# Optimization experiments

Measured on AMD Instinct MI355X. Metric: run time of the kernel, lower is better.

Reference implementation:

```python
import jax, jax.numpy as jnp
import numpy as np

R = 256        # residual channels
SKIP = 256     # skip channels
COND = 80      # conditioning (mel) channels
NUM_CLS = 256  # mu-law classes
T = 1024       # samples to generate
DILATIONS = tuple([1, 2, 4, 8, 16, 32, 64, 128, 256, 512] * 3)  # 30 layers, kernel_size=2
L = len(DILATIONS)


def setup_inputs() -> dict:
    key = jax.random.key(0)
    ks = jax.random.split(key, 15)
    sc = 0.05
    f = jnp.float32
    return {
        "y": jax.random.normal(ks[0], (COND, T), f),
        "emb": jnp.tanh(jax.random.normal(ks[1], (NUM_CLS, R), f)),  # buffer stores emb.tanh()
        "condition_W": jax.random.normal(ks[2], (L * 2 * R, COND), f) * sc,
        "WV_past": jax.random.normal(ks[3], (L, 2 * R, R), f) * sc,      # K=2 -> one past tap
        "WV_present": jax.random.normal(ks[4], (L, 2 * R, R), f) * sc,
        "W_o_weight": jax.random.normal(ks[5], (L - 1, R + SKIP, R), f) * sc,
        "W_o_bias": jax.random.normal(ks[6], (L - 1, R + SKIP), f) * sc,
        "W_o_weight_last": jax.random.normal(ks[7], (SKIP, R), f) * sc,
        "W_o_bias_last": jax.random.normal(ks[8], (SKIP,), f) * sc,
        "end1_w": jax.random.normal(ks[9], (SKIP, SKIP), f) * sc,
        "end1_b": jax.random.normal(ks[10], (SKIP,), f) * sc,
        "end2_w": jax.random.normal(ks[11], (NUM_CLS, SKIP), f) * sc,
        "end2_b": jax.random.normal(ks[12], (NUM_CLS,), f) * sc,
        "samples": jax.random.uniform(ks[13], (T,), f),  # torch.rand(T) inverse-CDF draws
    }


def _generate(y, emb, condition_W, WV_past, WV_present, W_o_weight, W_o_bias,
              W_o_weight_last, W_o_bias_last, end1_w, end1_b, end2_w, end2_b,
              samples, c=1.0):
    # all conditioning projections at once; chunked per layer as in torch.chunk(.., L, dim=0)
    conds_seq = (condition_W @ y).T.reshape(T, L, 2 * R)  # [T, L, 2R]
    x0 = emb[NUM_CLS // 2 - 1]
    mems0 = tuple(jnp.zeros((R, d), y.dtype) for d in DILATIONS)  # ring buffers per layer
    idx0 = jnp.zeros((L,), jnp.int32)

    def step(carry, inp):
        mems, idxs, x = carry
        cond_t, u = inp
        skip = jnp.zeros((SKIP,), x.dtype)
        new_mems, new_idxs = [], []
        for j in range(L):  # fixed small layer loop (structurally distinct buffers)
            mem, idx = mems[j], idxs[j]
            # kernel_size=2 -> single past tap read from ring buffer at idx
            h = cond_t[j] + WV_past[j] @ jnp.take(mem, idx, axis=1) + WV_present[j] @ x
            mem = mem.at[:, idx].set(x)  # write present sample, advance ring pointer
            new_mems.append(mem)
            new_idxs.append((idx + 1) % mem.shape[1])
            zw, zf = jnp.split(h, 2)
            z = jnp.tanh(zw) * jax.nn.sigmoid(zf)  # gated activation
            if j < L - 1:
                z2 = W_o_weight[j] @ z + W_o_bias[j]
                x = x + z2[:R]          # residual
                skip = skip + z2[R:]    # skip accumulation
            else:
                skip = skip + W_o_weight_last @ z + W_o_bias_last
        hid = jax.nn.relu(end1_w @ jax.nn.relu(skip) + end1_b)
        logits = (end2_w @ hid + end2_b) * c
        cum = jnp.cumsum(jax.nn.softmax(logits))
        new_idx = jnp.argmax(cum > u)  # first index with cum-prob > u  (inverse-CDF sample)
        return (tuple(new_mems), jnp.stack(new_idxs), emb[new_idx]), (new_idx, logits)

    _, (outputs, logits) = jax.lax.scan(step, (mems0, idx0, x0), (conds_seq, samples))
    return outputs.astype(jnp.int64), logits


def reference(y, emb, condition_W, WV_past, WV_present, W_o_weight, W_o_bias,
              W_o_weight_last, W_o_bias_last, end1_w, end1_b, end2_w, end2_b, samples):
    outputs, _ = _generate(y, emb, condition_W, WV_past, WV_present, W_o_weight,
                           W_o_bias, W_o_weight_last, W_o_bias_last,
                           end1_w, end1_b, end2_w, end2_b, samples)
    return outputs
```

## Files before the change

kernel.cpp:

```cpp
#include <hip/hip_runtime.h>
#include <stdint.h>


typedef unsigned long long u64;

#define TT 1024

#define OFF_PG   0
#define OFF_PS   (OFF_PG + 30*8*256*8)
#define OFF_XV   (OFF_PS + 30*8*256*8)
#define OFF_SB   (OFF_XV + 30*256*8)
#define OFF_HID  (OFF_SB + 30*256*8)
#define OFF_IDX  (OFF_HID + 256*8)
#define OFF_XH   (OFF_IDX + 64)
#define WS_NEED  ((size_t)OFF_XH + (size_t)30*1024*256*4)

__device__ __forceinline__ u64 ldp(const u64* p){
    return __hip_atomic_load((u64*)p, __ATOMIC_RELAXED, __HIP_MEMORY_SCOPE_AGENT);
}
__device__ __forceinline__ void stp(u64* p, float v, unsigned stamp){
    union { float f; unsigned u; } c; c.f = v;
    u64 w = ((u64)stamp << 32) | (u64)c.u;
    __hip_atomic_store(p, w, __ATOMIC_RELAXED, __HIP_MEMORY_SCOPE_AGENT);
}
__device__ __forceinline__ void stpu(u64* p, unsigned v, unsigned stamp){
    u64 w = ((u64)stamp << 32) | (u64)v;
    __hip_atomic_store(p, w, __ATOMIC_RELAXED, __HIP_MEMORY_SCOPE_AGENT);
}
__device__ __forceinline__ float pf(u64 w){
    union { unsigned u; float f; } c; c.u = (unsigned)(w & 0xffffffffu); return c.f;
}
__device__ __forceinline__ unsigned pstamp(u64 w){ return (unsigned)(w >> 32); }
__device__ __forceinline__ float ldf(const float* p){
    return __hip_atomic_load((float*)p, __ATOMIC_RELAXED, __HIP_MEMORY_SCOPE_AGENT);
}
__device__ __forceinline__ void stf(float* p, float v){
    __hip_atomic_store(p, v, __ATOMIC_RELAXED, __HIP_MEMORY_SCOPE_AGENT);
}
__device__ __forceinline__ long long rt(){
    return (long long)__builtin_amdgcn_s_memrealtime();
}
__device__ __forceinline__ void bar_lds(){
    asm volatile("s_waitcnt lgkmcnt(0)\n\ts_barrier" ::: "memory");
}

__global__ void __launch_bounds__(256, 1)
wavenet_v2(const float* __restrict__ gy,   const float* __restrict__ gemb,
           const float* __restrict__ gcw,  const float* __restrict__ gwvp,
           const float* __restrict__ gwvx, const float* __restrict__ gwo,
           const float* __restrict__ gwob, const float* __restrict__ gwol,
           const float* __restrict__ gwobl,const float* __restrict__ ge1w,
           const float* __restrict__ ge1b, const float* __restrict__ ge2w,
           const float* __restrict__ ge2b, const float* __restrict__ gsmp,
           float one, int* __restrict__ gout, char* __restrict__ ws)
{
    const int b = blockIdx.x, tid = threadIdx.x;
    const int xcd = b & 7, kk = b >> 3;
    const int jj = 4*xcd + (kk >> 3);
    const int cc = kk & 7;

    if (jj > 30 || (jj == 30 && cc > 2)) return;

    u64* PG   = (u64*)(ws + OFF_PG);
    u64* PS   = (u64*)(ws + OFF_PS);
    u64* XV   = (u64*)(ws + OFF_XV);
    u64* SB   = (u64*)(ws + OFF_SB);
    u64* HIDP = (u64*)(ws + OFF_HID);
    u64* IDXP = (u64*)(ws + OFF_IDX);
    float* xh = (float*)(ws + OFF_XH);

    __shared__ float sTap[256];
    __shared__ float sXin[256];
    __shared__ float sY[80];
    __shared__ float sZ[32];
    __shared__ float sred[8];
    __shared__ int   sidx[4];

    const long long ddl = rt() + 400000000LL;

    if (jj < 30){
        const int j   = jj;
        const int dil = 1 << (j % 10);
        const int q   = tid & 3;
        const int s   = (tid >> 2) & 15;
        const int w   = tid >> 6;
        const int gr  = (s < 8) ? (32*cc + 8*w + s)
                                : (256 + 32*cc + 8*w + (s - 8));

        const float* rw = (q < 2) ? (gwvp + ((size_t)j*512 + gr)*256 + 128*q)
                                  : (gwvx + ((size_t)j*512 + gr)*256 + 128*(q-2));
        float wv[128];
        #pragma unroll
        for (int i = 0; i < 32; i++){
            const int ci = (i + 2*q) & 31;
            wv[4*i+0] = rw[4*ci+0]*one; wv[4*i+1] = rw[4*ci+1]*one;
            wv[4*i+2] = rw[4*ci+2]*one; wv[4*i+3] = rw[4*ci+3]*one;
        }
        float cw[20];
        {
            const float* cp = gcw + ((size_t)(j*512 + gr))*80 + 20*q;
            #pragma unroll
            for (int i = 0; i < 20; i++) cw[i] = cp[i]*one;
        }
        float wo2[64]; float bres = 0.f, bskip = 0.f;
        if (j < 29){
            const float* w0 = gwo + ((size_t)j*512 + tid)*256 + 32*cc;
            const float* w1 = gwo + ((size_t)j*512 + 256 + tid)*256 + 32*cc;
            #pragma unroll
            for (int i = 0; i < 32; i++){ wo2[i] = w0[i]*one; wo2[32+i] = w1[i]*one; }
            bres  = gwob[j*512 + tid];
            bskip = gwob[j*512 + 256 + tid];
        } else {
            const float* w0 = gwol + (size_t)tid*256 + 32*cc;
            #pragma unroll
            for (int i = 0; i < 32; i++){ wo2[i] = w0[i]*one; wo2[32+i] = 0.f; }
            bskip = gwobl[tid];
        }

        u64* pgj = PG + (size_t)j*8*256;
        u64* psj = PS + (size_t)j*8*256;
        const u64* pgp = PG + (size_t)(j > 0 ? j-1 : 0)*8*256 + tid;
        const u64* psp = PS + (size_t)(j > 0 ? j-1 : 0)*8*256 + tid;
        const u64* xvp = XV + (size_t)(j > 0 ? j-1 : 0)*256 + tid;
        const u64* sbp = SB + (size_t)(j >= 2 ? j-1 : 0)*256 + tid;
        float* xhj = xh + (size_t)j*1024*256;
        float xv_prev = 0.f;

        for (int t = 0; t < TT; t++){
            const unsigned stamp = (unsigned)(t + 1);

            if (tid < 80) sY[tid] = gy[tid*TT + t];
            float tapv;
            if (dil == 1) tapv = xv_prev;
            else          tapv = (t >= dil) ? ldf(xhj + (size_t)(t-dil)*256 + tid) : 0.f;
            sTap[tid] = tapv;
            bar_lds();

            float acc = 0.f;
            #pragma unroll
            for (int i = 0; i < 20; i++) acc = fmaf(cw[i], sY[20*q + i], acc);
            if (q < 2){
                const float4* x4 = (const float4*)(sTap + 128*q);
                #pragma unroll
                for (int i = 0; i < 32; i++){
                    const int ci = (i + 2*q) & 31;
                    float4 v = x4[ci];
                    acc = fmaf(wv[4*i+0], v.x, acc); acc = fmaf(wv[4*i+1], v.y, acc);
                    acc = fmaf(wv[4*i+2], v.z, acc); acc = fmaf(wv[4*i+3], v.w, acc);
                }
            }

            float xv;
            if (j == 0){
                if (t == 0){
                    xv = gemb[127*256 + tid];
                } else {
                    u64 wIdx; int c = 0;
                    do {
                        wIdx = ldp(IDXP);
                        if (((++c) & 255) == 0 && rt() > ddl) break;
                    } while (pstamp(wIdx) != (unsigned)t);
                    const int idx = (int)(wIdx & 0xffffffffu) & 255;
                    xv = gemb[idx*256 + tid];
                }
            } else {
                u64 gwv[8]; u64 xvw = 0; u64 swv[8]; u64 sbw = 0;
                bool fresh; int c = 0;
                do {
                    #pragma unroll
                    for (int c2 = 0; c2 < 8; c2++) gwv[c2] = ldp(pgp + c2*256);
                    xvw = ldp(xvp);
                    bool ok = (pstamp(xvw) == stamp);
                    #pragma unroll
                    for (int c2 = 0; c2 < 8; c2++) ok &= (pstamp(gwv[c2]) == stamp);
                    if (cc == 0){
                        #pragma unroll
                        for (int c2 = 0; c2 < 8; c2++){
                            swv[c2] = ldp(psp + c2*256);
                            ok &= (pstamp(swv[c2]) == stamp);
                        }
                        if (j >= 2){ sbw = ldp(sbp); ok &= (pstamp(sbw) == stamp); }
                    }
                    fresh = ok;
                    if (((++c) & 255) == 0 && rt() > ddl) break;
                } while (!fresh);
                xv = pf(xvw);
                #pragma unroll
                for (int c2 = 0; c2 < 8; c2++) xv += pf(gwv[c2]);
                if (cc == 0){
                    float sv = (j >= 2) ? pf(sbw) : 0.f;
                    #pragma unroll
                    for (int c2 = 0; c2 < 8; c2++) sv += pf(swv[c2]);
                    stp(SB + (size_t)j*256 + tid, sv, stamp);
                }
            }
            xv_prev = xv;
            sXin[tid] = xv;
            if (cc == 0){
                stp(XV + (size_t)j*256 + tid, xv, stamp);
                if (dil > 1) stf(xhj + (size_t)t*256 + tid, xv);
            }
            bar_lds();

            if (q >= 2){
                const float4* x4 = (const float4*)(sXin + 128*(q-2));
                #pragma unroll
                for (int i = 0; i < 32; i++){
                    const int ci = (i + 2*q) & 31;
                    float4 v = x4[ci];
                    acc = fmaf(wv[4*i+0], v.x, acc); acc = fmaf(wv[4*i+1], v.y, acc);
                    acc = fmaf(wv[4*i+2], v.z, acc); acc = fmaf(wv[4*i+3], v.w, acc);
                }
            }
            acc += __shfl_xor(acc, 1, 64);
            acc += __shfl_xor(acc, 2, 64);
            const float hpart = __shfl_xor(acc, 32, 64);
            if (q == 0 && s < 8)
                sZ[8*w + s] = tanhf(acc) * (1.f/(1.f + expf(-hpart)));
            bar_lds();

            float g = 0.f, sk = 0.f;
            const float4* z4 = (const float4*)sZ;
            #pragma unroll
            for (int i = 0; i < 8; i++){
                float4 v = z4[i];
                g  = fmaf(wo2[4*i+0], v.x, g);  g  = fmaf(wo2[4*i+1], v.y, g);
                g  = fmaf(wo2[4*i+2], v.z, g);  g  = fmaf(wo2[4*i+3], v.w, g);
                sk = fmaf(wo2[32+4*i+0], v.x, sk); sk = fmaf(wo2[32+4*i+1], v.y, sk);
                sk = fmaf(wo2[32+4*i+2], v.z, sk); sk = fmaf(wo2[32+4*i+3], v.w, sk);
            }
            if (j < 29){
                if (cc == 0){ g += bres; sk += bskip; }
                stp(pgj + cc*256 + tid, g,  stamp);
                stp(psj + cc*256 + tid, sk, stamp);
            } else {
                if (cc == 0) g += bskip;
                stp(psj + cc*256 + tid, g, stamp);
            }
        }
        return;
    }

    if (jj == 30 && cc < 2){
        const int half = cc;
        const int r  = 128*half + (tid >> 1);
        const int hc = tid & 1;
        float e1[128];
        {
            const float* wp = ge1w + (size_t)r*256 + 128*hc;
            #pragma unroll
            for (int i = 0; i < 128; i++) e1[i] = wp[i]*one;
        }
        const float b1 = ge1b[r];
        const u64* psp = PS + (size_t)29*8*256 + tid;
        const u64* sbp = SB + (size_t)29*256 + tid;

        for (int t = 0; t < TT; t++){
            const unsigned stamp = (unsigned)(t + 1);
            u64 swv[8]; u64 sbw = 0; bool fresh; int c = 0;
            do {
                #pragma unroll
                for (int c2 = 0; c2 < 8; c2++) swv[c2] = ldp(psp + c2*256);
                sbw = ldp(sbp);
                bool ok = (pstamp(sbw) == stamp);
                #pragma unroll
                for (int c2 = 0; c2 < 8; c2++) ok &= (pstamp(swv[c2]) == stamp);
                fresh = ok;
                if (((++c) & 255) == 0 && rt() > ddl) break;
            } while (!fresh);
            float sk = pf(sbw);
            #pragma unroll
            for (int c2 = 0; c2 < 8; c2++) sk += pf(swv[c2]);
            sTap[tid] = fmaxf(sk, 0.f);
            bar_lds();
            float a = 0.f;
            const float4* p4 = (const float4*)(sTap + 128*hc);
            #pragma unroll
            for (int i = 0; i < 32; i++){
                float4 v = p4[i];
                a = fmaf(e1[4*i+0], v.x, a); a = fmaf(e1[4*i+1], v.y, a);
                a = fmaf(e1[4*i+2], v.z, a); a = fmaf(e1[4*i+3], v.w, a);
            }
            a += __shfl_xor(a, 1, 64);
            if (hc == 0) stp(HIDP + r, fmaxf(a + b1, 0.f), stamp);
            bar_lds();
        }
        return;
    }

    {
        float e2[256];
        {
            const float* wp = ge2w + (size_t)tid*256;
            #pragma unroll
            for (int i = 0; i < 256; i++) e2[i] = wp[i]*one;
        }
        const float b2 = ge2b[tid];
        const int w = tid >> 6, lane = tid & 63;

        for (int t = 0; t < TT; t++){
            const unsigned stamp = (unsigned)(t + 1);
            u64 hw; int c = 0;
            do {
                hw = ldp(HIDP + tid);
                if (((++c) & 255) == 0 && rt() > ddl) break;
            } while (pstamp(hw) != stamp);
            sTap[tid] = pf(hw);
            bar_lds();
            float a = b2;
            const float4* p4 = (const float4*)sTap;
            #pragma unroll
            for (int i = 0; i < 64; i++){
                float4 v = p4[i];
                a = fmaf(e2[4*i+0], v.x, a); a = fmaf(e2[4*i+1], v.y, a);
                a = fmaf(e2[4*i+2], v.z, a); a = fmaf(e2[4*i+3], v.w, a);
            }
            float m = a;
            #pragma unroll
            for (int off = 32; off > 0; off >>= 1) m = fmaxf(m, __shfl_xor(m, off, 64));
            if (lane == 0) sred[w] = m;
            bar_lds();
            m = fmaxf(fmaxf(sred[0], sred[1]), fmaxf(sred[2], sred[3]));
            float pe = expf(a - m);
            float ssum = pe;
            #pragma unroll
            for (int off = 32; off > 0; off >>= 1) ssum += __shfl_xor(ssum, off, 64);
            if (lane == 0) sred[4 + w] = ssum;
            bar_lds();
            const float S = sred[4] + sred[5] + sred[6] + sred[7];
            float cum = pe / S;
            #pragma unroll
            for (int off = 1; off < 64; off <<= 1){
                float vv = __shfl_up(cum, off, 64);
                if (lane >= off) cum += vv;
            }
            if (lane == 63) sred[w] = cum;
            bar_lds();
            float base = 0.f;
            if (w > 0) base += sred[0];
            if (w > 1) base += sred[1];
            if (w > 2) base += sred[2];
            cum += base;
            const float u = gsmp[t];
            unsigned long long bal = __ballot(cum > u);
            int cand = bal ? (w*64 + __ffsll((long long)bal) - 1) : (1 << 30);
            if (lane == 0) sidx[w] = cand;
            bar_lds();
            int idx = min(min(sidx[0], sidx[1]), min(sidx[2], sidx[3]));
            if (idx > 255) idx = 0;
            if (tid == 0){
                gout[t] = idx;
                stpu(IDXP, (unsigned)idx, stamp);
            }
            bar_lds();
        }
        return;
    }
}

__global__ void ws_too_small_kernel(int* out, int n){
    int i = blockIdx.x*256 + threadIdx.x;
    if (i < n) out[i] = 0;
}

extern "C" void kernel_launch(void* const* d_in, const int* in_sizes, int n_in,
                              void* d_out, int out_size, void* d_ws, size_t ws_size,
                              hipStream_t stream){
    (void)in_sizes; (void)n_in;
    if (ws_size < WS_NEED){
        hipLaunchKernelGGL(ws_too_small_kernel, dim3(4), dim3(256), 0, stream,
                           (int*)d_out, out_size);
        return;
    }
    hipLaunchKernelGGL(wavenet_v2, dim3(256), dim3(256), 0, stream,
                       (const float*)d_in[0],  (const float*)d_in[1],
                       (const float*)d_in[2],  (const float*)d_in[3],
                       (const float*)d_in[4],  (const float*)d_in[5],
                       (const float*)d_in[6],  (const float*)d_in[7],
                       (const float*)d_in[8],  (const float*)d_in[9],
                       (const float*)d_in[10], (const float*)d_in[11],
                       (const float*)d_in[12], (const float*)d_in[13],
                       1.0f, (int*)d_out, (char*)d_ws);
}
```

Measured before the change: 108.6 ms.

## Add atomic-RMW fast-path channel for inter-block handoff with timed fallback

Adds a second set of stamped mailboxes, placed in unused history slots of the workspace. Producers now also write them with atomic exchange, and consumers poll them with fetch_add(0) at workgroup scope. Each wait first spins on this fast channel for a short realtime window, and only then falls back to the original relaxed agent-scope polling. The fast path stays enabled only if it hit at least once in the first 24 steps. The aim is to cut per-layer handoff latency on the serial sample chain. The cost is extra atomic stores on every write, and a possible timeout penalty on every step if workgroup-scope atomics are not visible across XCDs.

```diff
diff --git a/kernel.cpp b/kernel.cpp
--- a/kernel.cpp
+++ b/kernel.cpp
@@ -15,6 +15,9 @@
 #define OFF_XH   (OFF_IDX + 64)
 #define WS_NEED  ((size_t)OFF_XH + (size_t)30*1024*256*4)
 
+
+#define FAST_TO  320
+
 __device__ __forceinline__ u64 ldp(const u64* p){
     return __hip_atomic_load((u64*)p, __ATOMIC_RELAXED, __HIP_MEMORY_SCOPE_AGENT);
 }
@@ -44,8 +47,20 @@
     asm volatile("s_waitcnt lgkmcnt(0)\n\ts_barrier" ::: "memory");
 }
 
+__device__ __forceinline__ u64 fld(const u64* p, u64 z){
+    return __hip_atomic_fetch_add((u64*)p, z,
+                                  __ATOMIC_RELAXED, __HIP_MEMORY_SCOPE_WORKGROUP);
+}
+__device__ __forceinline__ void fst(u64* p, u64 w){
+    (void)__hip_atomic_exchange(p, w, __ATOMIC_RELAXED, __HIP_MEMORY_SCOPE_WORKGROUP);
+}
+__device__ __forceinline__ u64 pk(float v, unsigned stamp){
+    union { float f; unsigned u; } c; c.f = v;
+    return ((u64)stamp << 32) | (u64)c.u;
+}
+
 __global__ void __launch_bounds__(256, 1)
-wavenet_v2(const float* __restrict__ gy,   const float* __restrict__ gemb,
+wavenet_v6(const float* __restrict__ gy,   const float* __restrict__ gemb,
            const float* __restrict__ gcw,  const float* __restrict__ gwvp,
            const float* __restrict__ gwvx, const float* __restrict__ gwo,
            const float* __restrict__ gwob, const float* __restrict__ gwol,
@@ -69,6 +84,18 @@
     u64* IDXP = (u64*)(ws + OFF_IDX);
     float* xh = (float*)(ws + OFF_XH);
 
+    u64* FPG  = (u64*)(ws + OFF_XH);
+    u64* FPS  = FPG + 30*8*256;
+    u64* F2   = (u64*)(ws + OFF_XH + (size_t)10*1024*256*4);
+    u64* FXV  = F2;
+    u64* FSB  = FXV + 30*256;
+    u64* FHID = FSB + 30*256;
+    u64* FIDX = FHID + 256;
+
+    unsigned zr = 0u;
+    asm volatile("" : "+v"(zr));
+    const u64 z64 = (u64)zr;
+
     __shared__ float sTap[256];
     __shared__ float sXin[256];
     __shared__ float sY[80];
@@ -117,14 +144,21 @@
             bskip = gwobl[tid];
         }
 
-        u64* pgj = PG + (size_t)j*8*256;
-        u64* psj = PS + (size_t)j*8*256;
-        const u64* pgp = PG + (size_t)(j > 0 ? j-1 : 0)*8*256 + tid;
-        const u64* psp = PS + (size_t)(j > 0 ? j-1 : 0)*8*256 + tid;
-        const u64* xvp = XV + (size_t)(j > 0 ? j-1 : 0)*256 + tid;
-        const u64* sbp = SB + (size_t)(j >= 2 ? j-1 : 0)*256 + tid;
+        u64* pgj  = PG  + (size_t)j*8*256;
+        u64* psj  = PS  + (size_t)j*8*256;
+        u64* fpgj = FPG + (size_t)j*8*256;
+        u64* fpsj = FPS + (size_t)j*8*256;
+        const u64* pgp  = PG  + (size_t)(j > 0 ? j-1 : 0)*8*256 + tid;
+        const u64* psp  = PS  + (size_t)(j > 0 ? j-1 : 0)*8*256 + tid;
+        const u64* xvp  = XV  + (size_t)(j > 0 ? j-1 : 0)*256 + tid;
+        const u64* sbp  = SB  + (size_t)(j >= 2 ? j-1 : 0)*256 + tid;
+        const u64* fpgp = FPG + (size_t)(j > 0 ? j-1 : 0)*8*256 + tid;
+        const u64* fpsp = FPS + (size_t)(j > 0 ? j-1 : 0)*8*256 + tid;
+        const u64* fxvp = FXV + (size_t)(j > 0 ? j-1 : 0)*256 + tid;
+        const u64* fsbp = FSB + (size_t)(j >= 2 ? j-1 : 0)*256 + tid;
         float* xhj = xh + (size_t)j*1024*256;
         float xv_prev = 0.f;
+        int fh = 0;
 
         for (int t = 0; t < TT; t++){
             const unsigned stamp = (unsigned)(t + 1);
@@ -155,35 +189,70 @@
                 if (t == 0){
                     xv = gemb[127*256 + tid];
                 } else {
-                    u64 wIdx; int c = 0;
-                    do {
-                        wIdx = ldp(IDXP);
-                        if (((++c) & 255) == 0 && rt() > ddl) break;
-                    } while (pstamp(wIdx) != (unsigned)t);
+                    u64 wIdx = 0; bool hit = false;
+                    if (t < 24 || fh > 0){
+                        const long long tf = rt() + FAST_TO;
+                        do {
+                            wIdx = fld(FIDX, z64);
+                            hit = (pstamp(wIdx) == (unsigned)t);
+                        } while (!hit && rt() < tf);
+                        if (hit) fh++;
+                    }
+                    if (!hit){
+                        int c = 0;
+                        do {
+                            wIdx = ldp(IDXP);
+                            if (((++c) & 255) == 0 && rt() > ddl) break;
+                        } while (pstamp(wIdx) != (unsigned)t);
+                    }
                     const int idx = (int)(wIdx & 0xffffffffu) & 255;
                     xv = gemb[idx*256 + tid];
                 }
             } else {
                 u64 gwv[8]; u64 xvw = 0; u64 swv[8]; u64 sbw = 0;
-                bool fresh; int c = 0;
-                do {
-                    #pragma unroll
-                    for (int c2 = 0; c2 < 8; c2++) gwv[c2] = ldp(pgp + c2*256);
-                    xvw = ldp(xvp);
-                    bool ok = (pstamp(xvw) == stamp);
-                    #pragma unroll
-                    for (int c2 = 0; c2 < 8; c2++) ok &= (pstamp(gwv[c2]) == stamp);
-                    if (cc == 0){
+                bool hit = false;
+                if (t < 24 || fh > 0){
+                    const long long tf = rt() + FAST_TO;
+                    do {
                         #pragma unroll
-                        for (int c2 = 0; c2 < 8; c2++){
-                            swv[c2] = ldp(psp + c2*256);
-                            ok &= (pstamp(swv[c2]) == stamp);
+                        for (int c2 = 0; c2 < 8; c2++) gwv[c2] = fld(fpgp + c2*256, z64);
+                        xvw = fld(fxvp, z64);
+                        bool ok = (pstamp(xvw) == stamp);
+                        #pragma unroll
+                        for (int c2 = 0; c2 < 8; c2++) ok &= (pstamp(gwv[c2]) == stamp);
+                        if (cc == 0){
+                            #pragma unroll
+                            for (int c2 = 0; c2 < 8; c2++){
+                                swv[c2] = fld(fpsp + c2*256, z64);
+                                ok &= (pstamp(swv[c2]) == stamp);
+                            }
+                            if (j >= 2){ sbw = fld(fsbp, z64); ok &= (pstamp(sbw) == stamp); }
                         }
-                        if (j >= 2){ sbw = ldp(sbp); ok &= (pstamp(sbw) == stamp); }
-                    }
-                    fresh = ok;
-                    if (((++c) & 255) == 0 && rt() > ddl) break;
-                } while (!fresh);
+                        hit = ok;
+                    } while (!hit && rt() < tf);
+                    if (hit) fh++;
+                }
+                if (!hit){
+                    bool fresh; int c = 0;
+                    do {
+                        #pragma unroll
+                        for (int c2 = 0; c2 < 8; c2++) gwv[c2] = ldp(pgp + c2*256);
+                        xvw = ldp(xvp);
+                        bool ok = (pstamp(xvw) == stamp);
+                        #pragma unroll
+                        for (int c2 = 0; c2 < 8; c2++) ok &= (pstamp(gwv[c2]) == stamp);
+                        if (cc == 0){
+                            #pragma unroll
+                            for (int c2 = 0; c2 < 8; c2++){
+                                swv[c2] = ldp(psp + c2*256);
+                                ok &= (pstamp(swv[c2]) == stamp);
+                            }
+                            if (j >= 2){ sbw = ldp(sbp); ok &= (pstamp(sbw) == stamp); }
+                        }
+                        fresh = ok;
+                        if (((++c) & 255) == 0 && rt() > ddl) break;
+                    } while (!fresh);
+                }
                 xv = pf(xvw);
                 #pragma unroll
                 for (int c2 = 0; c2 < 8; c2++) xv += pf(gwv[c2]);
@@ -191,12 +260,14 @@
                     float sv = (j >= 2) ? pf(sbw) : 0.f;
                     #pragma unroll
                     for (int c2 = 0; c2 < 8; c2++) sv += pf(swv[c2]);
+                    fst(FSB + (size_t)j*256 + tid, pk(sv, stamp));
                     stp(SB + (size_t)j*256 + tid, sv, stamp);
                 }
             }
             xv_prev = xv;
             sXin[tid] = xv;
             if (cc == 0){
+                fst(FXV + (size_t)j*256 + tid, pk(xv, stamp));
                 stp(XV + (size_t)j*256 + tid, xv, stamp);
                 if (dil > 1) stf(xhj + (size_t)t*256 + tid, xv);
             }
@@ -231,10 +302,13 @@
             }
             if (j < 29){
                 if (cc == 0){ g += bres; sk += bskip; }
+                fst(fpgj + cc*256 + tid, pk(g,  stamp));
+                fst(fpsj + cc*256 + tid, pk(sk, stamp));
                 stp(pgj + cc*256 + tid, g,  stamp);
                 stp(psj + cc*256 + tid, sk, stamp);
             } else {
                 if (cc == 0) g += bskip;
+                fst(fpsj + cc*256 + tid, pk(g, stamp));
                 stp(psj + cc*256 + tid, g, stamp);
             }
         }
@@ -252,22 +326,41 @@
             for (int i = 0; i < 128; i++) e1[i] = wp[i]*one;
         }
         const float b1 = ge1b[r];
-        const u64* psp = PS + (size_t)29*8*256 + tid;
-        const u64* sbp = SB + (size_t)29*256 + tid;
+        const u64* psp  = PS  + (size_t)29*8*256 + tid;
+        const u64* sbp  = SB  + (size_t)29*256 + tid;
+        const u64* fpsp = FPS + (size_t)29*8*256 + tid;
+        const u64* fsbp = FSB + (size_t)29*256 + tid;
+        int fh = 0;
 
         for (int t = 0; t < TT; t++){
             const unsigned stamp = (unsigned)(t + 1);
-            u64 swv[8]; u64 sbw = 0; bool fresh; int c = 0;
-            do {
-                #pragma unroll
-                for (int c2 = 0; c2 < 8; c2++) swv[c2] = ldp(psp + c2*256);
-                sbw = ldp(sbp);
-                bool ok = (pstamp(sbw) == stamp);
-                #pragma unroll
-                for (int c2 = 0; c2 < 8; c2++) ok &= (pstamp(swv[c2]) == stamp);
-                fresh = ok;
-                if (((++c) & 255) == 0 && rt() > ddl) break;
-            } while (!fresh);
+            u64 swv[8]; u64 sbw = 0; bool hit = false;
+            if (t < 24 || fh > 0){
+                const long long tf = rt() + FAST_TO;
+                do {
+                    #pragma unroll
+                    for (int c2 = 0; c2 < 8; c2++) swv[c2] = fld(fpsp + c2*256, z64);
+                    sbw = fld(fsbp, z64);
+                    bool ok = (pstamp(sbw) == stamp);
+                    #pragma unroll
+                    for (int c2 = 0; c2 < 8; c2++) ok &= (pstamp(swv[c2]) == stamp);
+                    hit = ok;
+                } while (!hit && rt() < tf);
+                if (hit) fh++;
+            }
+            if (!hit){
+                bool fresh; int c = 0;
+                do {
+                    #pragma unroll
+                    for (int c2 = 0; c2 < 8; c2++) swv[c2] = ldp(psp + c2*256);
+                    sbw = ldp(sbp);
+                    bool ok = (pstamp(sbw) == stamp);
+                    #pragma unroll
+                    for (int c2 = 0; c2 < 8; c2++) ok &= (pstamp(swv[c2]) == stamp);
+                    fresh = ok;
+                    if (((++c) & 255) == 0 && rt() > ddl) break;
+                } while (!fresh);
+            }
             float sk = pf(sbw);
             #pragma unroll
             for (int c2 = 0; c2 < 8; c2++) sk += pf(swv[c2]);
@@ -282,7 +375,11 @@
                 a = fmaf(e1[4*i+2], v.z, a); a = fmaf(e1[4*i+3], v.w, a);
             }
             a += __shfl_xor(a, 1, 64);
-            if (hc == 0) stp(HIDP + r, fmaxf(a + b1, 0.f), stamp);
+            if (hc == 0){
+                const float hv = fmaxf(a + b1, 0.f);
+                fst(FHID + r, pk(hv, stamp));
+                stp(HIDP + r, hv, stamp);
+            }
             bar_lds();
         }
         return;
@@ -297,14 +394,26 @@
         }
         const float b2 = ge2b[tid];
         const int w = tid >> 6, lane = tid & 63;
+        int fh = 0;
 
         for (int t = 0; t < TT; t++){
             const unsigned stamp = (unsigned)(t + 1);
-            u64 hw; int c = 0;
-            do {
-                hw = ldp(HIDP + tid);
-                if (((++c) & 255) == 0 && rt() > ddl) break;
-            } while (pstamp(hw) != stamp);
+            u64 hw = 0; bool hit = false;
+            if (t < 24 || fh > 0){
+                const long long tf = rt() + FAST_TO;
+                do {
+                    hw = fld(FHID + tid, z64);
+                    hit = (pstamp(hw) == stamp);
+                } while (!hit && rt() < tf);
+                if (hit) fh++;
+            }
+            if (!hit){
+                int c = 0;
+                do {
+                    hw = ldp(HIDP + tid);
+                    if (((++c) & 255) == 0 && rt() > ddl) break;
+                } while (pstamp(hw) != stamp);
+            }
             sTap[tid] = pf(hw);
             bar_lds();
             float a = b2;
@@ -350,6 +459,7 @@
             if (idx > 255) idx = 0;
             if (tid == 0){
                 gout[t] = idx;
+                fst(FIDX, ((u64)stamp << 32) | (u64)(unsigned)idx);
                 stpu(IDXP, (unsigned)idx, stamp);
             }
             bar_lds();
@@ -372,7 +482,7 @@
                            (int*)d_out, out_size);
         return;
     }
-    hipLaunchKernelGGL(wavenet_v2, dim3(256), dim3(256), 0, stream,
+    hipLaunchKernelGGL(wavenet_v6, dim3(256), dim3(256), 0, stream,
                        (const float*)d_in[0],  (const float*)d_in[1],
                        (const float*)d_in[2],  (const float*)d_in[3],
                        (const float*)d_in[4],  (const float*)d_in[5],
```

Result: slower. 114.5 ms (+5.5%).
